# Optimization experiments

Measured on AMD Instinct MI355X. Metric: run time of the kernel, lower is better.

Reference implementation:

```python
import jax, jax.numpy as jnp
import numpy as np

NPOINT = 1024
RADIUS = 0.4
NSAMPLE = 32
BN_EPS = 1e-3  # keras BatchNormalization default epsilon


def _fps(xyz, npoint):
    # xyz: [N,3] -> indices [npoint] via farthest point sampling (seed index 0)
    N = xyz.shape[0]

    def step(carry, _):
        dists, far = carry
        d = jnp.sum((xyz - xyz[far]) ** 2, axis=-1)
        dists = jnp.minimum(dists, d)
        return (dists, jnp.argmax(dists).astype(jnp.int32)), far

    init = (jnp.full((N,), 1e10, dtype=xyz.dtype), jnp.asarray(0, dtype=jnp.int32))
    _, idx = jax.lax.scan(step, init, None, length=npoint)
    return idx


def _ball_query(xyz, new_xyz, radius, nsample):
    # xyz: [N,3], new_xyz: [S,3] -> idx [S,nsample]
    # First up-to-nsample points (in original index order) within radius of each
    # center; slots past the count are filled with the first found index
    # (matching the CUDA query_ball_point semantics).
    N = xyz.shape[0]
    d2 = jnp.sum((new_xyz[:, None, :] - xyz[None, :, :]) ** 2, axis=-1)  # [S,N]
    key = jnp.where(d2 < radius * radius, jnp.arange(N, dtype=jnp.int32), N)
    sk = jnp.sort(key, axis=-1)[:, :nsample]          # first valid indices, padded with N
    first = sk[:, :1]
    first = jnp.where(first < N, first, 0)            # fallback if no neighbor found
    idx = jnp.where(sk < N, sk, first)
    return idx.astype(jnp.int32)


def _gather(pts, idx):
    # pts: [B,N,C], idx: [B,...] -> [B,...,C]
    return jax.vmap(lambda p, i: p[i])(pts, idx)


def _conv_bn_relu(x, W, b, g, be):
    # 1x1 conv over [B,P,S,Cin] + batchnorm (training mode, batch stats) + relu
    y = jnp.einsum('bpsc,co->bpso', x, W) + b
    m = jnp.mean(y, axis=(0, 1, 2))
    v = jnp.var(y, axis=(0, 1, 2))
    y = (y - m) * jax.lax.rsqrt(v + BN_EPS) * g + be
    return jax.nn.relu(y)


def setup_inputs() -> dict:
    key = jax.random.key(0)
    ks = jax.random.split(key, 8)
    B, N, C = 16, 4096, 64
    xyz = jax.random.normal(ks[0], (B, N, 3), dtype=jnp.float32)
    points = jax.random.normal(ks[1], (B, N, C), dtype=jnp.float32)
    chans = [3 + C, 64, 64, 128]
    inp = {'xyz': xyz, 'points': points}
    for i in range(3):
        cin, cout = chans[i], chans[i + 1]
        limit = np.sqrt(6.0 / (cin + cout))  # glorot uniform
        inp[f'W{i}'] = jax.random.uniform(ks[2 + i], (cin, cout), jnp.float32, -limit, limit)
        inp[f'b{i}'] = jnp.zeros((cout,), jnp.float32)
        inp[f'g{i}'] = jnp.ones((cout,), jnp.float32)
        inp[f'be{i}'] = jnp.zeros((cout,), jnp.float32)
    return inp


def reference(xyz, points, W0, b0, g0, be0, W1, b1, g1, be1, W2, b2, g2, be2):
    xyz_c = jax.lax.stop_gradient(xyz)
    fps_idx = jax.vmap(lambda p: _fps(p, NPOINT))(xyz_c)           # [B,NPOINT]
    new_xyz = _gather(xyz, fps_idx)                                 # [B,NPOINT,3]
    idx = jax.vmap(lambda p, c: _ball_query(p, c, RADIUS, NSAMPLE))(
        xyz_c, jax.lax.stop_gradient(new_xyz))                      # [B,NPOINT,NSAMPLE]
    grouped_xyz = _gather(xyz, idx) - new_xyz[:, :, None, :]        # centered local coords
    grouped_points = _gather(points, idx)                           # [B,NPOINT,NSAMPLE,C]
    new_points = jnp.concatenate([grouped_xyz, grouped_points], axis=-1)
    new_points = _conv_bn_relu(new_points, W0, b0, g0, be0)
    new_points = _conv_bn_relu(new_points, W1, b1, g1, be1)
    new_points = _conv_bn_relu(new_points, W2, b2, g2, be2)
    new_points = jnp.max(new_points, axis=2)                        # max-pool over nsample
    return (new_xyz, new_points, idx)
```

## Files before the change

### kernel.cpp

```cpp
#include <hip/hip_runtime.h>

static constexpr int NB      = 16;
static constexpr int NPTS    = 4096;
static constexpr int NPOINTS = 1024;
static constexpr int NSAMP   = 32;
static constexpr int CIN0    = 67;
static constexpr int C0      = 64;
static constexpr int C1      = 64;
static constexpr int C2      = 128;
static constexpr size_t MROWS = (size_t)NB * NPOINTS * NSAMP;
#define RAD2 0.16f
#define BN_EPS 0.001f

__device__ __forceinline__ float4 uld4(const float* __restrict__ p) {
    return *(const float4* __restrict__)p;
}

__device__ __forceinline__ unsigned short f2bf(float f) {
    const unsigned u = __float_as_uint(f);
    return (unsigned short)((u + 0x7fffu + ((u >> 16) & 1u)) >> 16);
}
__device__ __forceinline__ float bf2f(unsigned short h) {
    return __uint_as_float((unsigned)h << 16);
}

template<int CTRL>
__device__ __forceinline__ float dppf(float v) {
    return __int_as_float(__builtin_amdgcn_update_dpp(0, __float_as_int(v),
                                                      CTRL, 0xF, 0xF, false));
}
template<int CTRL>
__device__ __forceinline__ float dpps(float v) {
    return __int_as_float(__builtin_amdgcn_update_dpp(__float_as_int(v), __float_as_int(v),
                                                      CTRL, 0xF, 0xF, false));
}
__device__ __forceinline__ float dpp_sum64(float v) {
    v += dppf<0x111>(v); v += dppf<0x112>(v); v += dppf<0x114>(v); v += dppf<0x118>(v);
    v += dppf<0x142>(v); v += dppf<0x143>(v);
    return v;
}
__device__ __forceinline__ float dpp_max32(float v) {
    v = fmaxf(v, dpps<0x111>(v)); v = fmaxf(v, dpps<0x112>(v));
    v = fmaxf(v, dpps<0x114>(v)); v = fmaxf(v, dpps<0x118>(v));
    v = fmaxf(v, dpps<0x142>(v));
    return v;
}
__device__ __forceinline__ float dpp_min32(float v) {
    v = fminf(v, dpps<0x111>(v)); v = fminf(v, dpps<0x112>(v));
    v = fminf(v, dpps<0x114>(v)); v = fminf(v, dpps<0x118>(v));
    v = fminf(v, dpps<0x142>(v));
    return v;
}
template<int CTRL>
__device__ __forceinline__ void kstep(unsigned long long& k) {
    const unsigned hi = (unsigned)(k >> 32);
    const unsigned lo = (unsigned)(k & 0xffffffffull);
    const unsigned ohi = (unsigned)__builtin_amdgcn_update_dpp((int)hi, (int)hi, CTRL, 0xF, 0xF, false);
    const unsigned olo = (unsigned)__builtin_amdgcn_update_dpp((int)lo, (int)lo, CTRL, 0xF, 0xF, false);
    const unsigned long long ok = ((unsigned long long)ohi << 32) | olo;
    if (ok > k) k = ok;
}

__global__ __launch_bounds__(512) void fps_kernel(const float* __restrict__ xyz,
                                                  float* __restrict__ out_newxyz)
{
    __shared__ float sx[NPTS], sy[NPTS], sz[NPTS];
    __shared__ int   sidx[NPOINTS];
    __shared__ __align__(16) unsigned long long redk[2][8];

    const int b    = blockIdx.x;
    const int tid  = threadIdx.x;
    const int lane = tid & 63;
    const int wv   = tid >> 6;

    const float* base = xyz + (size_t)b * NPTS * 3;
    for (int i = tid; i < NPTS; i += 512) {
        sx[i] = base[i * 3 + 0];
        sy[i] = base[i * 3 + 1];
        sz[i] = base[i * 3 + 2];
    }
    __syncthreads();

    float px[8], py[8], pz[8], dd[8];
#pragma unroll
    for (int j = 0; j < 8; ++j) {
        const int i = tid + j * 512;
        px[j] = sx[i]; py[j] = sy[i]; pz[j] = sz[i];
        dd[j] = 1e10f;
    }

    int   far = 0;
    float fx = sx[0], fy = sy[0], fz = sz[0];
#pragma unroll 1
    for (int it = 0; it < NPOINTS; ++it) {
        if (tid == 0) sidx[it] = far;
        float bv = -1.0f; int bi = 0;
#pragma unroll
        for (int j = 0; j < 8; ++j) {
            const float dx = __fsub_rn(px[j], fx);
            const float dy = __fsub_rn(py[j], fy);
            const float dz = __fsub_rn(pz[j], fz);
            const float d  = __fadd_rn(__fadd_rn(__fmul_rn(dx, dx), __fmul_rn(dy, dy)),
                                       __fmul_rn(dz, dz));
            dd[j] = fminf(dd[j], d);
            if (dd[j] > bv) { bv = dd[j]; bi = tid + j * 512; }
        }
        unsigned long long k = ((unsigned long long)__float_as_uint(bv) << 32)
                             | (unsigned)(4095 - bi);
        kstep<0x111>(k);
        kstep<0x112>(k);
        kstep<0x114>(k);
        kstep<0x118>(k);
        kstep<0x142>(k);
        kstep<0x143>(k);

        const int pb = it & 1;
        if (lane == 63) redk[pb][wv] = k;
        __syncthreads();
// ... 5 lines not shown
        }
        const int ci = 4095 - (int)(unsigned)(ck & 0xffffffffull);
        far = ci;
        fx = sx[ci]; fy = sy[ci]; fz = sz[ci];
    }
    __syncthreads();
    for (int it = tid; it < NPOINTS; it += 512) {
        const int ii = sidx[it];
        float* o = out_newxyz + ((size_t)b * NPOINTS + it) * 3;
        o[0] = sx[ii]; o[1] = sy[ii]; o[2] = sz[ii];
    }
}

__global__ __launch_bounds__(256) void ball_kernel(const float* __restrict__ xyz,
                                                   const float* __restrict__ newxyz,
                                                   float* __restrict__ out_idx_f)
{
    __shared__ int sel[4][NSAMP];
    const int tid  = threadIdx.x;
    const int lane = tid & 63;
    const int widx = tid >> 6;
    const int w = blockIdx.x * 4 + widx;
    const int b = w >> 10;

    const float cx = newxyz[(size_t)w * 3 + 0];
    const float cy = newxyz[(size_t)w * 3 + 1];
    const float cz = newxyz[(size_t)w * 3 + 2];
    const float* base = xyz + (size_t)b * NPTS * 3;

    int total = 0;
    for (int c = 0; c < NPTS / 64 && total < NSAMP; ++c) {
        const int n = c * 64 + lane;
        const float dx = __fsub_rn(cx, base[n * 3 + 0]);
        const float dy = __fsub_rn(cy, base[n * 3 + 1]);
        const float dz = __fsub_rn(cz, base[n * 3 + 2]);
        const float d2 = __fadd_rn(__fadd_rn(__fmul_rn(dx, dx), __fmul_rn(dy, dy)),
                                   __fmul_rn(dz, dz));
        const bool pred = d2 < RAD2;
        const unsigned long long mask = __ballot(pred);
        if (pred) {
            const int pos = total + (int)__popcll(mask & ((1ull << lane) - 1ull));
            if (pos < NSAMP) sel[widx][pos] = n;
        }
        total += (int)__popcll(mask);
    }
    __syncthreads();
    if (lane < NSAMP) {
        const int first = sel[widx][0];
        const int v = (lane < total) ? sel[widx][lane] : first;
        out_idx_f[(size_t)w * NSAMP + lane] = (float)v;
    }
}

__device__ __forceinline__ void stats4(float a0, float a1, float a2, float a3,
                                       float* sa, int lane)
{
    float q0 = a0*a0, q1 = a1*a1, q2 = a2*a2, q3 = a3*a3;
    a0 = dpp_sum64(a0); q0 = dpp_sum64(q0);
    a1 = dpp_sum64(a1); q1 = dpp_sum64(q1);
    a2 = dpp_sum64(a2); q2 = dpp_sum64(q2);
    a3 = dpp_sum64(a3); q3 = dpp_sum64(q3);
    if (lane == 63) {
        sa[0] += a0; sa[1] += q0; sa[2] += a1; sa[3] += q1;
        sa[4] += a2; sa[5] += q2; sa[6] += a3; sa[7] += q3;
    }
}

__global__ __launch_bounds__(256) void preP_kernel(const float* __restrict__ points,
                                                   const float* __restrict__ W0,
                                                   float* __restrict__ P)
{
    const int r = blockIdx.x * 256 + threadIdx.x;
    const float4* pr = (const float4*)(points + (size_t)r * 64);
    float x[64];
#pragma unroll
    for (int j = 0; j < 16; ++j) {
        const float4 v = pr[j];
        x[4*j+0] = v.x; x[4*j+1] = v.y; x[4*j+2] = v.z; x[4*j+3] = v.w;
    }
    float acc[64];
#pragma unroll
    for (int o = 0; o < 64; ++o) acc[o] = 0.f;
#pragma unroll 2
    for (int k = 0; k < 64; ++k) {
        const float xk = x[k];
#pragma unroll
        for (int oc = 0; oc < 16; ++oc) {
            const float4 w4 = uld4(W0 + (3 + k) * 64 + 4 * oc);
            acc[4*oc+0] = fmaf(xk, w4.x, acc[4*oc+0]);
            acc[4*oc+1] = fmaf(xk, w4.y, acc[4*oc+1]);
            acc[4*oc+2] = fmaf(xk, w4.z, acc[4*oc+2]);
            acc[4*oc+3] = fmaf(xk, w4.w, acc[4*oc+3]);
        }
    }
    float4* po = (float4*)(P + (size_t)r * 64);
#pragma unroll
    for (int oc = 0; oc < 16; ++oc)
        po[oc] = make_float4(acc[4*oc+0], acc[4*oc+1], acc[4*oc+2], acc[4*oc+3]);
}

__device__ __forceinline__ void layer0_dedup(
    const float* __restrict__ xyz, const float* __restrict__ P,
    const float* __restrict__ newxyz, const float* __restrict__ idxf,
    const float* __restrict__ W0, const float* __restrict__ b0,
    int r, float* x1)
{
    const int i  = (int)idxf[r];
    const int bb = r >> 15;
    const int pp = (r >> 5) & 1023;
    const float* pz = xyz + ((size_t)bb * NPTS + i) * 3;
    const float* nz = newxyz + ((size_t)bb * NPOINTS + pp) * 3;
    const float r0 = pz[0] - nz[0];
    const float r1 = pz[1] - nz[1];
    const float r2 = pz[2] - nz[2];
    const float4* prow = (const float4*)(P + ((size_t)bb * NPTS + i) * 64);
#pragma unroll
    for (int oc = 0; oc < 16; ++oc) {
        const float4 pv = prow[oc];
        const float4 bv = uld4(b0 + 4 * oc);
        const float4 wa = uld4(W0 + 0 * 64 + 4 * oc);
        const float4 wb = uld4(W0 + 1 * 64 + 4 * oc);
        const float4 wc = uld4(W0 + 2 * 64 + 4 * oc);
        x1[4*oc+0] = fmaf(r0, wa.x, fmaf(r1, wb.x, fmaf(r2, wc.x, bv.x + pv.x)));
        x1[4*oc+1] = fmaf(r0, wa.y, fmaf(r1, wb.y, fmaf(r2, wc.y, bv.y + pv.y)));
        x1[4*oc+2] = fmaf(r0, wa.z, fmaf(r1, wb.z, fmaf(r2, wc.z, bv.z + pv.z)));
        x1[4*oc+3] = fmaf(r0, wa.w, fmaf(r1, wb.w, fmaf(r2, wc.w, bv.w + pv.w)));
    }
}

template<int PHASE>
__global__ __launch_bounds__(256, 2) void passP_kernel(
    const float* __restrict__ xyz, const float* __restrict__ P,
    const float* __restrict__ newxyz, const float* __restrict__ idxf,
    const float* __restrict__ W0, const float* __restrict__ b0,
    const float* __restrict__ W1, const float* __restrict__ b1,
    const float* __restrict__ W2, const float* __restrict__ b2,
    const float* __restrict__ ss0, const float* __restrict__ ss1,
    const float* __restrict__ ss2,
    float* __restrict__ gstats, float* __restrict__ out_np)
{
    constexpr int CS = (PHASE == 2) ? C2 : C0;
    __shared__ float sacc[4][2 * CS];

    const int tid  = threadIdx.x;
    const int lane = tid & 63;
    const int wv   = tid >> 6;

    if constexpr (PHASE <= 2) {
        for (int j = tid; j < 8 * CS; j += 256) (&sacc[0][0])[j] = 0.f;
        __syncthreads();
    }

    const int r = blockIdx.x * 256 + tid;
    float x1[C0];
    layer0_dedup(xyz, P, newxyz, idxf, W0, b0, r, x1);

    if constexpr (PHASE == 0) {
#pragma unroll
        for (int oc = 0; oc < 16; ++oc)
            stats4(x1[4*oc+0], x1[4*oc+1], x1[4*oc+2], x1[4*oc+3], &sacc[wv][8*oc], lane);
    } else {
#pragma unroll
        for (int o = 0; o < C0; ++o)
            x1[o] = fmaxf(0.f, fmaf(x1[o], ss0[o], ss0[64 + o]));

        float y1[C1];
#pragma unroll
        for (int o = 0; o < C1; o += 4) {
            const float4 bv = uld4(b1 + o);
            y1[o] = bv.x; y1[o+1] = bv.y; y1[o+2] = bv.z; y1[o+3] = bv.w;
        }
#pragma unroll 2
        for (int k = 0; k < C0; ++k) {
            const float xk = x1[k];
#pragma unroll
            for (int oc = 0; oc < 16; ++oc) {
                const float4 w4 = uld4(W1 + k * 64 + 4 * oc);
                y1[4*oc+0] = fmaf(xk, w4.x, y1[4*oc+0]);
                y1[4*oc+1] = fmaf(xk, w4.y, y1[4*oc+1]);
                y1[4*oc+2] = fmaf(xk, w4.z, y1[4*oc+2]);
                y1[4*oc+3] = fmaf(xk, w4.w, y1[4*oc+3]);
            }
// ... 3 lines not shown
#pragma unroll
            for (int oc = 0; oc < 16; ++oc)
                stats4(y1[4*oc+0], y1[4*oc+1], y1[4*oc+2], y1[4*oc+3], &sacc[wv][8*oc], lane);
        } else {
#pragma unroll
            for (int o = 0; o < C1; ++o)
                y1[o] = fmaxf(0.f, fmaf(y1[o], ss1[o], ss1[64 + o]));

            float a2[C2];
#pragma unroll
            for (int o = 0; o < C2; o += 4) {
                const float4 bv = uld4(b2 + o);
                a2[o] = bv.x; a2[o+1] = bv.y; a2[o+2] = bv.z; a2[o+3] = bv.w;
            }
#pragma unroll 2
            for (int k = 0; k < C1; ++k) {
                const float xk = y1[k];
#pragma unroll
                for (int o = 0; o < C2; o += 4) {
                    const float4 w4 = uld4(W2 + k * C2 + o);
                    a2[o+0] = fmaf(xk, w4.x, a2[o+0]);
                    a2[o+1] = fmaf(xk, w4.y, a2[o+1]);
                    a2[o+2] = fmaf(xk, w4.z, a2[o+2]);
                    a2[o+3] = fmaf(xk, w4.w, a2[o+3]);
                }
            }

            if constexpr (PHASE == 2) {
#pragma unroll
                for (int o = 0; o < C2; ++o) {
                    const float s = dpp_sum64(a2[o]);
                    const float q = dpp_sum64(a2[o] * a2[o]);
                    if (lane == 63) { sacc[wv][2*o] += s; sacc[wv][2*o+1] += q; }
                }
            } else {
                const int g = r >> 5;
#pragma unroll
                for (int o = 0; o < C2; ++o) {
                    float v = fmaxf(0.f, fmaf(a2[o], ss2[o], ss2[C2 + o]));
                    v = dpp_max32(v);
                    if (lane == 31 || lane == 63) out_np[(size_t)g * C2 + o] = v;
                }
            }
        }
    }

    if constexpr (PHASE <= 2) {
        __syncthreads();
        for (int j = tid; j < 2 * CS; j += 256)
            atomicAdd(&gstats[j], sacc[0][j] + sacc[1][j] + sacc[2][j] + sacc[3][j]);
    }
}

__global__ __launch_bounds__(256, 2) void pass1Y_kernel(
    const float* __restrict__ xyz, const float* __restrict__ P,
    const float* __restrict__ newxyz, const float* __restrict__ idxf,
    const float* __restrict__ W0, const float* __restrict__ b0,
    const float* __restrict__ W1, const float* __restrict__ b1,
    const float* __restrict__ ss0,
    float* __restrict__ gstats, unsigned short* __restrict__ y1b)
{
    __shared__ float sacc[4][2 * C0];

    const int tid  = threadIdx.x;
    const int lane = tid & 63;
    const int wv   = tid >> 6;

    for (int j = tid; j < 8 * C0; j += 256) (&sacc[0][0])[j] = 0.f;
    __syncthreads();

    const int r = blockIdx.x * 256 + tid;
    float x1[C0];
    layer0_dedup(xyz, P, newxyz, idxf, W0, b0, r, x1);
#pragma unroll
    for (int o = 0; o < C0; ++o)
        x1[o] = fmaxf(0.f, fmaf(x1[o], ss0[o], ss0[64 + o]));

    float y1[C1];
#pragma unroll
    for (int o = 0; o < C1; o += 4) {
        const float4 bv = uld4(b1 + o);
        y1[o] = bv.x; y1[o+1] = bv.y; y1[o+2] = bv.z; y1[o+3] = bv.w;
    }
#pragma unroll 2
    for (int k = 0; k < C0; ++k) {
        const float xk = x1[k];
#pragma unroll
        for (int oc = 0; oc < 16; ++oc) {
            const float4 w4 = uld4(W1 + k * 64 + 4 * oc);
            y1[4*oc+0] = fmaf(xk, w4.x, y1[4*oc+0]);
            y1[4*oc+1] = fmaf(xk, w4.y, y1[4*oc+1]);
            y1[4*oc+2] = fmaf(xk, w4.z, y1[4*oc+2]);
            y1[4*oc+3] = fmaf(xk, w4.w, y1[4*oc+3]);
        }
    }

#pragma unroll
    for (int oc = 0; oc < 16; ++oc)
        stats4(y1[4*oc+0], y1[4*oc+1], y1[4*oc+2], y1[4*oc+3], &sacc[wv][8*oc], lane);

    uint4* yo = (uint4*)(y1b + (size_t)r * 64);
#pragma unroll
    for (int gq = 0; gq < 8; ++gq) {
        union { unsigned short u[8]; uint4 v; } pk;
#pragma unroll
        for (int e = 0; e < 8; ++e) pk.u[e] = f2bf(y1[8*gq+e]);
        yo[gq] = pk.v;
    }

    __syncthreads();
    for (int j = tid; j < 2 * C0; j += 256)
        atomicAdd(&gstats[j], sacc[0][j] + sacc[1][j] + sacc[2][j] + sacc[3][j]);
}

__global__ __launch_bounds__(256, 2) void p2Y_kernel(
    const unsigned short* __restrict__ y1b,
    const float* __restrict__ W2, const float* __restrict__ b2,
    const float* __restrict__ ss1,
    float* __restrict__ gstats, float* __restrict__ mnmx)
{
    __shared__ float sacc[4][2 * C2];

    const int tid  = threadIdx.x;
    const int lane = tid & 63;
    const int wv   = tid >> 6;

    for (int j = tid; j < 8 * C2; j += 256) (&sacc[0][0])[j] = 0.f;
    __syncthreads();

    const int r = blockIdx.x * 256 + tid;

    float y1[C1];
    {
        const uint4* yi = (const uint4*)(y1b + (size_t)r * 64);
#pragma unroll
        for (int gq = 0; gq < 8; ++gq) {
            union { uint4 v; unsigned short u[8]; } pk;
            pk.v = yi[gq];
#pragma unroll
            for (int e = 0; e < 8; ++e)
                y1[8*gq+e] = bf2f(pk.u[e]);
        }
    }
#pragma unroll
    for (int o = 0; o < C1; ++o)
        y1[o] = fmaxf(0.f, fmaf(y1[o], ss1[o], ss1[64 + o]));

    float a2[C2];
#pragma unroll
    for (int o = 0; o < C2; o += 4) {
        const float4 bv = uld4(b2 + o);
        a2[o] = bv.x; a2[o+1] = bv.y; a2[o+2] = bv.z; a2[o+3] = bv.w;
    }
#pragma unroll 2
    for (int k = 0; k < C1; ++k) {
        const float xk = y1[k];
#pragma unroll
        for (int o = 0; o < C2; o += 4) {
            const float4 w4 = uld4(W2 + k * C2 + o);
            a2[o+0] = fmaf(xk, w4.x, a2[o+0]);
            a2[o+1] = fmaf(xk, w4.y, a2[o+1]);
            a2[o+2] = fmaf(xk, w4.z, a2[o+2]);
            a2[o+3] = fmaf(xk, w4.w, a2[o+3]);
        }
    }

    const int gbase = blockIdx.x * 8 + 2 * wv;
    float* mb = mnmx + ((size_t)gbase + (lane >> 5)) * 256;
#pragma unroll
    for (int o = 0; o < C2; ++o) {
        const float v = a2[o];
        const float s = dpp_sum64(v);
        const float q = dpp_sum64(v * v);
        const float mn = dpp_min32(v);
        const float mx = dpp_max32(v);
        if (lane == 63) { sacc[wv][2*o] += s; sacc[wv][2*o+1] += q; }
        if (lane == 31 || lane == 63) { mb[o] = mn; mb[128 + o] = mx; }
    }

    __syncthreads();
    for (int j = tid; j < 2 * C2; j += 256)
        atomicAdd(&gstats[j], sacc[0][j] + sacc[1][j] + sacc[2][j] + sacc[3][j]);
}

__global__ __launch_bounds__(256, 2) void passP2mm_kernel(
    const float* __restrict__ xyz, const float* __restrict__ P,
    const float* __restrict__ newxyz, const float* __restrict__ idxf,
    const float* __restrict__ W0, const float* __restrict__ b0,
    const float* __restrict__ W1, const float* __restrict__ b1,
    const float* __restrict__ W2, const float* __restrict__ b2,
    const float* __restrict__ ss0, const float* __restrict__ ss1,
    float* __restrict__ gstats, float* __restrict__ mnmx)
{
    __shared__ float sacc[4][2 * C2];

    const int tid  = threadIdx.x;
    const int lane = tid & 63;
    const int wv   = tid >> 6;

    for (int j = tid; j < 8 * C2; j += 256) (&sacc[0][0])[j] = 0.f;
    __syncthreads();

    const int r = blockIdx.x * 256 + tid;
    float x1[C0];
    layer0_dedup(xyz, P, newxyz, idxf, W0, b0, r, x1);
#pragma unroll
    for (int o = 0; o < C0; ++o)
        x1[o] = fmaxf(0.f, fmaf(x1[o], ss0[o], ss0[64 + o]));

    float y1[C1];
#pragma unroll
    for (int o = 0; o < C1; o += 4) {
        const float4 bv = uld4(b1 + o);
        y1[o] = bv.x; y1[o+1] = bv.y; y1[o+2] = bv.z; y1[o+3] = bv.w;
    }
#pragma unroll 2
    for (int k = 0; k < C0; ++k) {
        const float xk = x1[k];
#pragma unroll
        for (int oc = 0; oc < 16; ++oc) {
            const float4 w4 = uld4(W1 + k * 64 + 4 * oc);
            y1[4*oc+0] = fmaf(xk, w4.x, y1[4*oc+0]);
            y1[4*oc+1] = fmaf(xk, w4.y, y1[4*oc+1]);
            y1[4*oc+2] = fmaf(xk, w4.z, y1[4*oc+2]);
            y1[4*oc+3] = fmaf(xk, w4.w, y1[4*oc+3]);
        }
    }
#pragma unroll
    for (int o = 0; o < C1; ++o)
        y1[o] = fmaxf(0.f, fmaf(y1[o], ss1[o], ss1[64 + o]));

    float a2[C2];
#pragma unroll
    for (int o = 0; o < C2; o += 4) {
        const float4 bv = uld4(b2 + o);
        a2[o] = bv.x; a2[o+1] = bv.y; a2[o+2] = bv.z; a2[o+3] = bv.w;
    }
#pragma unroll 2
    for (int k = 0; k < C1; ++k) {
        const float xk = y1[k];
#pragma unroll
        for (int o = 0; o < C2; o += 4) {
            const float4 w4 = uld4(W2 + k * C2 + o);
            a2[o+0] = fmaf(xk, w4.x, a2[o+0]);
            a2[o+1] = fmaf(xk, w4.y, a2[o+1]);
            a2[o+2] = fmaf(xk, w4.z, a2[o+2]);
            a2[o+3] = fmaf(xk, w4.w, a2[o+3]);
        }
    }

    const int gbase = blockIdx.x * 8 + 2 * wv;
    float* mb = mnmx + ((size_t)gbase + (lane >> 5)) * 256;
#pragma unroll
    for (int o = 0; o < C2; ++o) {
        const float v = a2[o];
        const float s = dpp_sum64(v);
        const float q = dpp_sum64(v * v);
        const float mn = dpp_min32(v);
        const float mx = dpp_max32(v);
        if (lane == 63) { sacc[wv][2*o] += s; sacc[wv][2*o+1] += q; }
        if (lane == 31 || lane == 63) { mb[o] = mn; mb[128 + o] = mx; }
    }

    __syncthreads();
    for (int j = tid; j < 2 * C2; j += 256)
        atomicAdd(&gstats[j], sacc[0][j] + sacc[1][j] + sacc[2][j] + sacc[3][j]);
}

__global__ __launch_bounds__(256) void fin_kernel(const float* __restrict__ mnmx,
                                                  const float* __restrict__ ss2,
                                                  float* __restrict__ out_np)
{
    const int t = blockIdx.x * 256 + threadIdx.x;
    const int g = t >> 7;
    const int o = t & 127;
    const float sc = ss2[o], sh = ss2[C2 + o];
    const float y  = (sc >= 0.f) ? mnmx[(size_t)g * 256 + 128 + o]
                                 : mnmx[(size_t)g * 256 + o];
    out_np[t] = fmaxf(0.f, fmaf(y, sc, sh));
}

template<int PHASE>
__global__ __launch_bounds__(128) void pass_kernel(
    const float* __restrict__ xyz, const float* __restrict__ points,
    const float* __restrict__ newxyz, const float* __restrict__ idxf,
    const float* __restrict__ W0, const float* __restrict__ b0,
    const float* __restrict__ W1, const float* __restrict__ b1,
    const float* __restrict__ W2, const float* __restrict__ b2,
    const float* __restrict__ ss0, const float* __restrict__ ss1,
    const float* __restrict__ ss2,
    float* __restrict__ gstats, float* __restrict__ out_np)
{
    constexpr int CS = (PHASE == 2) ? C2 : C0;
    __shared__ float xld[(PHASE >= 1) ? (64 * 128) : 1];
    __shared__ float sacc[2][2 * CS];

    const int tid  = threadIdx.x;
    const int lane = tid & 63;
    const int wv   = tid >> 6;

    if constexpr (PHASE <= 2) {
        for (int j = tid; j < 2 * 2 * CS; j += 128) (&sacc[0][0])[j] = 0.f;
        __syncthreads();
    }

    const int r  = blockIdx.x * 128 + tid;
    const int i  = (int)idxf[r];
    const int bb = r >> 15;
    const int pp = (r >> 5) & 1023;

    float x[CIN0];
    {
        const float* pz = xyz + ((size_t)bb * NPTS + i) * 3;
        const float* nz = newxyz + ((size_t)bb * NPOINTS + pp) * 3;
        x[0] = pz[0] - nz[0];
        x[1] = pz[1] - nz[1];
        x[2] = pz[2] - nz[2];
        const float4* p4 = (const float4*)(points + ((size_t)bb * NPTS + i) * 64);
#pragma unroll
        for (int j = 0; j < 16; ++j) {
            const float4 v = p4[j];
            x[3+4*j+0] = v.x; x[3+4*j+1] = v.y; x[3+4*j+2] = v.z; x[3+4*j+3] = v.w;
        }
    }

#pragma unroll 1
    for (int oc = 0; oc < 16; ++oc) {
        const float4 bv = uld4(b0 + 4*oc);
        float a0 = bv.x, a1 = bv.y, a2 = bv.z, a3 = bv.w;
#pragma unroll
        for (int k = 0; k < CIN0; ++k) {
            const float4 w4 = uld4(W0 + k*64 + 4*oc);
            a0 = fmaf(x[k], w4.x, a0); a1 = fmaf(x[k], w4.y, a1);
            a2 = fmaf(x[k], w4.z, a2); a3 = fmaf(x[k], w4.w, a3);
// ... 33 lines not shown
        }
#pragma unroll 1
        for (int oc = 0; oc < 16; ++oc) {
            const float4 bv = uld4(b1 + 4*oc);
            float a0 = bv.x, a1 = bv.y, a2 = bv.z, a3 = bv.w;
#pragma unroll
            for (int k = 0; k < 64; ++k) {
                const float xk = xld[k*128 + tid];
                const float4 w4 = uld4(W1 + k*64 + 4*oc);
                a0 = fmaf(xk, w4.x, a0); a1 = fmaf(xk, w4.y, a1);
                a2 = fmaf(xk, w4.z, a2); a3 = fmaf(xk, w4.w, a3);
            }
            const float xc0 = fmaxf(0.f, fmaf(a0, ss1[4*oc+0], ss1[64+4*oc+0]));
            const float xc1 = fmaxf(0.f, fmaf(a1, ss1[4*oc+1], ss1[64+4*oc+1]));
            const float xc2 = fmaxf(0.f, fmaf(a2, ss1[4*oc+2], ss1[64+4*oc+2]));
            const float xc3 = fmaxf(0.f, fmaf(a3, ss1[4*oc+3], ss1[64+4*oc+3]));
#pragma unroll
            for (int o = 0; o < C2; o += 4) {
                const float4 wA = uld4(W2 + (4*oc+0)*C2 + o);
                const float4 wB = uld4(W2 + (4*oc+1)*C2 + o);
                const float4 wC = uld4(W2 + (4*oc+2)*C2 + o);
                const float4 wD = uld4(W2 + (4*oc+3)*C2 + o);
                acc2[o+0] = fmaf(xc0, wA.x, fmaf(xc1, wB.x, fmaf(xc2, wC.x, fmaf(xc3, wD.x, acc2[o+0]))));
                acc2[o+1] = fmaf(xc0, wA.y, fmaf(xc1, wB.y, fmaf(xc2, wC.y, fmaf(xc3, wD.y, acc2[o+1]))));
                acc2[o+2] = fmaf(xc0, wA.z, fmaf(xc1, wB.z, fmaf(xc2, wC.z, fmaf(xc3, wD.z, acc2[o+2]))));
                acc2[o+3] = fmaf(xc0, wA.w, fmaf(xc1, wB.w, fmaf(xc2, wC.w, fmaf(xc3, wD.w, acc2[o+3]))));
            }
        }

        if constexpr (PHASE == 2) {
#pragma unroll
            for (int o = 0; o < C2; ++o) {
                const float s = dpp_sum64(acc2[o]);
                const float q = dpp_sum64(acc2[o] * acc2[o]);
                if (lane == 63) { sacc[wv][2*o] += s; sacc[wv][2*o+1] += q; }
            }
        } else {
            const int g = r >> 5;
#pragma unroll
            for (int o = 0; o < C2; ++o) {
                float v = fmaxf(0.f, fmaf(acc2[o], ss2[o], ss2[C2+o]));
                v = dpp_max32(v);
                if (lane == 31 || lane == 63) out_np[(size_t)g * C2 + o] = v;
            }
        }
    }

    if constexpr (PHASE <= 2) {
        __syncthreads();
        for (int j = tid; j < 2 * CS; j += 128)
            atomicAdd(&gstats[j], sacc[0][j] + sacc[1][j]);
    }
}

template<int C>
__global__ void ss_kernel(const float* __restrict__ gs, const float* __restrict__ g,
                          const float* __restrict__ be, float* __restrict__ ss)
{
    const int o = threadIdx.x;
    const float inv  = 1.0f / (float)MROWS;
    const float mean = gs[2*o] * inv;
    const float var  = fmaxf(0.f, gs[2*o+1] * inv - mean * mean);
    const float sc   = g[o] / sqrtf(var + BN_EPS);
    ss[o]     = sc;
    ss[C + o] = fmaf(-mean, sc, be[o]);
}

__global__ void zero_kernel(float* __restrict__ p) { p[threadIdx.x] = 0.f; }

extern "C" void kernel_launch(void* const* d_in, const int* in_sizes, int n_in,
                              void* d_out, int out_size, void* d_ws, size_t ws_size,
                              hipStream_t stream)
{
    (void)in_sizes; (void)n_in; (void)out_size;
    const float* xyz    = (const float*)d_in[0];
    const float* points = (const float*)d_in[1];
    const float* W0  = (const float*)d_in[2];
    const float* b0  = (const float*)d_in[3];
    const float* g0  = (const float*)d_in[4];
    const float* be0 = (const float*)d_in[5];
    const float* W1  = (const float*)d_in[6];
    const float* b1  = (const float*)d_in[7];
    const float* g1  = (const float*)d_in[8];
    const float* be1 = (const float*)d_in[9];
    const float* W2  = (const float*)d_in[10];
    const float* b2  = (const float*)d_in[11];
    const float* g2  = (const float*)d_in[12];
    const float* be2 = (const float*)d_in[13];

    float* out = (float*)d_out;
    float* out_newxyz = out;
    float* out_newpts = out + (size_t)NB * NPOINTS * 3;
    float* out_idx    = out_newpts + (size_t)NB * NPOINTS * C2;

    float* wsf = (float*)d_ws;
    float* gs0 = wsf + 0;
    float* gs1 = wsf + 128;
    float* gs2 = wsf + 256;
    float* ss0 = wsf + 512;
    float* ss1 = wsf + 640;
    float* ss2 = wsf + 768;
    const size_t PBYTES  = (size_t)NB * NPTS * C0 * 4;
    const size_t MMBYTES = (size_t)NB * NPOINTS * 2 * C2 * 4;
    const size_t YBYTES  = MROWS * C1 * 2;
    float* P    = (float*)((char*)d_ws + 65536);
    float* mnmx = (float*)((char*)d_ws + 65536 + PBYTES);
    unsigned short* y1b = (unsigned short*)((char*)d_ws + 65536 + PBYTES + MMBYTES);

    const bool haveP  = ws_size >= (65536 + PBYTES);
    const bool haveMM = ws_size >= (65536 + PBYTES + MMBYTES);
    const bool haveY  = ws_size >= (65536 + PBYTES + MMBYTES + YBYTES);

    zero_kernel<<<1, 512, 0, stream>>>(wsf);
    fps_kernel<<<NB, 512, 0, stream>>>(xyz, out_newxyz);
    ball_kernel<<<(NB * NPOINTS) / 4, 256, 0, stream>>>(xyz, out_newxyz, out_idx);

    if (haveP) {
        const int grid = (int)(MROWS / 256);
        preP_kernel<<<NB * NPTS / 256, 256, 0, stream>>>(points, W0, P);
        passP_kernel<0><<<grid, 256, 0, stream>>>(xyz, P, out_newxyz, out_idx,
                                                  W0, b0, W1, b1, W2, b2,
                                                  ss0, ss1, ss2, gs0, nullptr);
        ss_kernel<C0><<<1, C0, 0, stream>>>(gs0, g0, be0, ss0);
        if (haveY) {
            pass1Y_kernel<<<grid, 256, 0, stream>>>(xyz, P, out_newxyz, out_idx,
                                                    W0, b0, W1, b1, ss0, gs1, y1b);
            ss_kernel<C1><<<1, C1, 0, stream>>>(gs1, g1, be1, ss1);
            p2Y_kernel<<<grid, 256, 0, stream>>>(y1b, W2, b2, ss1, gs2, mnmx);
            ss_kernel<C2><<<1, C2, 0, stream>>>(gs2, g2, be2, ss2);
            fin_kernel<<<NB * NPOINTS * C2 / 256, 256, 0, stream>>>(mnmx, ss2, out_newpts);
        } else if (haveMM) {
            passP_kernel<1><<<grid, 256, 0, stream>>>(xyz, P, out_newxyz, out_idx,
                                                      W0, b0, W1, b1, W2, b2,
                                                      ss0, ss1, ss2, gs1, nullptr);
            ss_kernel<C1><<<1, C1, 0, stream>>>(gs1, g1, be1, ss1);
            passP2mm_kernel<<<grid, 256, 0, stream>>>(xyz, P, out_newxyz, out_idx,
                                                      W0, b0, W1, b1, W2, b2,
                                                      ss0, ss1, gs2, mnmx);
            ss_kernel<C2><<<1, C2, 0, stream>>>(gs2, g2, be2, ss2);
            fin_kernel<<<NB * NPOINTS * C2 / 256, 256, 0, stream>>>(mnmx, ss2, out_newpts);
        } else {
            passP_kernel<1><<<grid, 256, 0, stream>>>(xyz, P, out_newxyz, out_idx,
                                                      W0, b0, W1, b1, W2, b2,
                                                      ss0, ss1, ss2, gs1, nullptr);
            ss_kernel<C1><<<1, C1, 0, stream>>>(gs1, g1, be1, ss1);
            passP_kernel<2><<<grid, 256, 0, stream>>>(xyz, P, out_newxyz, out_idx,
                                                      W0, b0, W1, b1, W2, b2,
                                                      ss0, ss1, ss2, gs2, nullptr);
            ss_kernel<C2><<<1, C2, 0, stream>>>(gs2, g2, be2, ss2);
            passP_kernel<3><<<grid, 256, 0, stream>>>(xyz, P, out_newxyz, out_idx,
                                                      W0, b0, W1, b1, W2, b2,
                                                      ss0, ss1, ss2, nullptr, out_newpts);
        }
    } else {
        const int grid = (int)(MROWS / 128);
        pass_kernel<0><<<grid, 128, 0, stream>>>(xyz, points, out_newxyz, out_idx,
                                                 W0, b0, W1, b1, W2, b2,
                                                 ss0, ss1, ss2, gs0, nullptr);
        ss_kernel<C0><<<1, C0, 0, stream>>>(gs0, g0, be0, ss0);
        pass_kernel<1><<<grid, 128, 0, stream>>>(xyz, points, out_newxyz, out_idx,
                                                 W0, b0, W1, b1, W2, b2,
                                                 ss0, ss1, ss2, gs1, nullptr);
        ss_kernel<C1><<<1, C1, 0, stream>>>(gs1, g1, be1, ss1);
        pass_kernel<2><<<grid, 128, 0, stream>>>(xyz, points, out_newxyz, out_idx,
                                                 W0, b0, W1, b1, W2, b2,
                                                 ss0, ss1, ss2, gs2, nullptr);
        ss_kernel<C2><<<1, C2, 0, stream>>>(gs2, g2, be2, ss2);
        pass_kernel<3><<<grid, 128, 0, stream>>>(xyz, points, out_newxyz, out_idx,
                                                 W0, b0, W1, b1, W2, b2,
                                                 ss0, ss1, ss2, nullptr, out_newpts);
    }
}
```

Measured before the change: 1.286 ms.

## Fold preP and zeroing into FPS launch, inline BN scale, partial-sum stats

Runs the zeroing and the per-point W0 projection (P) as extra blocks inside the FPS launch, so they overlap the latency-bound FPS blocks instead of running as separate launches. Drops the tiny ss_kernel launches by computing the BN scale and shift inline at the start of each pass and in the final kernel. Adds a dedicated pass0 kernel that only collects layer-0 stats. Replaces the full-wave DPP sums with 8-lane partial sums written to a padded shared array, which removes the shared-memory zeroing and the read-modify-write accumulation. p2Y now splits the 128 output channels into two 64-wide halves to reduce register pressure, and occupancy hints are raised from 2 to 3 or 4 blocks. Costs include redundant BN recomputation per block and the risk of spills from the higher occupancy targets.

```diff
diff --git a/kernel.cpp b/kernel.cpp
--- a/kernel.cpp
+++ b/kernel.cpp
@@ -39,6 +39,14 @@
     v += dppf<0x142>(v); v += dppf<0x143>(v);
     return v;
 }
+__device__ __forceinline__ float dpp_psum8(float v) {
+    v += dppf<0x111>(v); v += dppf<0x112>(v); v += dppf<0x114>(v);
+    return v;
+}
+__device__ __forceinline__ float dpp_psum16(float v) {
+    v += dppf<0x111>(v); v += dppf<0x112>(v); v += dppf<0x114>(v); v += dppf<0x118>(v);
+    return v;
+}
 __device__ __forceinline__ float dpp_max32(float v) {
     v = fmaxf(v, dpps<0x111>(v)); v = fmaxf(v, dpps<0x112>(v));
     v = fmaxf(v, dpps<0x114>(v)); v = fmaxf(v, dpps<0x118>(v));
@@ -62,8 +70,47 @@
 }
 
 __global__ __launch_bounds__(512) void fps_kernel(const float* __restrict__ xyz,
-                                                  float* __restrict__ out_newxyz)
-{
+                                                  float* __restrict__ out_newxyz,
+                                                  float* __restrict__ wsz,
+                                                  const float* __restrict__ points,
+                                                  const float* __restrict__ W0,
+                                                  float* __restrict__ P)
+{
+    if (blockIdx.x == NB) {
+        for (int i = threadIdx.x; i < 1024; i += 512) wsz[i] = 0.f;
+        return;
+    }
+    if (blockIdx.x > NB) {
+        const int r = (blockIdx.x - NB - 1) * 512 + threadIdx.x;
+        const float4* pr = (const float4*)(points + (size_t)r * 64);
+        float x[64];
+#pragma unroll
+        for (int j = 0; j < 16; ++j) {
+            const float4 v = pr[j];
+            x[4*j+0] = v.x; x[4*j+1] = v.y; x[4*j+2] = v.z; x[4*j+3] = v.w;
+        }
+        float acc[64];
+#pragma unroll
+        for (int o = 0; o < 64; ++o) acc[o] = 0.f;
+#pragma unroll 2
+        for (int k = 0; k < 64; ++k) {
+            const float xk = x[k];
+#pragma unroll
+            for (int oc = 0; oc < 16; ++oc) {
+                const float4 w4 = uld4(W0 + (3 + k) * 64 + 4 * oc);
+                acc[4*oc+0] = fmaf(xk, w4.x, acc[4*oc+0]);
+                acc[4*oc+1] = fmaf(xk, w4.y, acc[4*oc+1]);
+                acc[4*oc+2] = fmaf(xk, w4.z, acc[4*oc+2]);
+                acc[4*oc+3] = fmaf(xk, w4.w, acc[4*oc+3]);
+            }
+        }
+        float4* po = (float4*)(P + (size_t)r * 64);
+#pragma unroll
+        for (int oc = 0; oc < 16; ++oc)
+            po[oc] = make_float4(acc[4*oc+0], acc[4*oc+1], acc[4*oc+2], acc[4*oc+3]);
+        return;
+    }
+
     __shared__ float sx[NPTS], sy[NPTS], sz[NPTS];
     __shared__ int   sidx[NPOINTS];
     __shared__ __align__(16) unsigned long long redk[2][8];
@@ -175,6 +222,20 @@
     }
 }
 
+__device__ __forceinline__ void stats4q8(float a0, float a1, float a2, float a3,
+                                         float2* sa, bool wr)
+{
+    float q0 = a0*a0, q1 = a1*a1, q2 = a2*a2, q3 = a3*a3;
+    a0 = dpp_psum8(a0); q0 = dpp_psum8(q0);
+    a1 = dpp_psum8(a1); q1 = dpp_psum8(q1);
+    a2 = dpp_psum8(a2); q2 = dpp_psum8(q2);
+    a3 = dpp_psum8(a3); q3 = dpp_psum8(q3);
+    if (wr) {
+        *(float4*)&sa[0] = make_float4(a0, q0, a1, q1);
+        *(float4*)&sa[2] = make_float4(a2, q2, a3, q3);
+    }
+}
+
 __device__ __forceinline__ void stats4(float a0, float a1, float a2, float a3,
                                        float* sa, int lane)
 {
@@ -251,6 +312,237 @@
     }
 }
 
+template<int C>
+__device__ __forceinline__ void bn_inline(const float* __restrict__ gs,
+                                          const float* __restrict__ g,
+                                          const float* __restrict__ be,
+                                          float* ssl, int tid)
+{
+    if (tid < C) {
+        const float inv  = 1.0f / (float)MROWS;
+        const float mean = gs[2*tid] * inv;
+        const float var  = fmaxf(0.f, gs[2*tid+1] * inv - mean * mean);
+        const float sc   = g[tid] / sqrtf(var + BN_EPS);
+        ssl[tid]     = sc;
+        ssl[C + tid] = fmaf(-mean, sc, be[tid]);
+    }
+}
+
+__global__ __launch_bounds__(256, 4) void pass0_kernel(
+    const float* __restrict__ xyz, const float* __restrict__ P,
+    const float* __restrict__ newxyz, const float* __restrict__ idxf,
+    const float* __restrict__ W0, const float* __restrict__ b0,
+    float* __restrict__ gstats)
+{
+    __shared__ float2 sacc[32][C0 + 1];
+    const int tid  = threadIdx.x;
+    const int lane = tid & 63;
+    const int wv   = tid >> 6;
+    const int slot = wv * 8 + (lane >> 3);
+    const bool wr  = (lane & 7) == 7;
+
+    const int r = blockIdx.x * 256 + tid;
+    float x1[C0];
+    layer0_dedup(xyz, P, newxyz, idxf, W0, b0, r, x1);
+
+#pragma unroll
+    for (int oc = 0; oc < 16; ++oc)
+        stats4q8(x1[4*oc+0], x1[4*oc+1], x1[4*oc+2], x1[4*oc+3], &sacc[slot][4*oc], wr);
+
+    __syncthreads();
+    for (int j = tid; j < C0; j += 256) {
+        float s = 0.f, q = 0.f;
+#pragma unroll
+        for (int v = 0; v < 32; ++v) { s += sacc[v][j].x; q += sacc[v][j].y; }
+        atomicAdd(&gstats[2*j], s);
+        atomicAdd(&gstats[2*j+1], q);
+    }
+}
+
+__global__ __launch_bounds__(256, 3) void pass1Y_kernel(
+    const float* __restrict__ xyz, const float* __restrict__ P,
+    const float* __restrict__ newxyz, const float* __restrict__ idxf,
+    const float* __restrict__ W0, const float* __restrict__ b0,
+    const float* __restrict__ W1, const float* __restrict__ b1,
+    const float* __restrict__ gs0, const float* __restrict__ g0,
+    const float* __restrict__ be0,
+    float* __restrict__ gstats, unsigned short* __restrict__ y1b)
+{
+    __shared__ float2 sacc[32][C0 + 1];
+    __shared__ float ssl[2 * C0];
+    const int tid  = threadIdx.x;
+    const int lane = tid & 63;
+    const int wv   = tid >> 6;
+    const int slot = wv * 8 + (lane >> 3);
+    const bool wr  = (lane & 7) == 7;
+
+    bn_inline<C0>(gs0, g0, be0, ssl, tid);
+    __syncthreads();
+
+    const int r = blockIdx.x * 256 + tid;
+    float x1[C0];
+    layer0_dedup(xyz, P, newxyz, idxf, W0, b0, r, x1);
+#pragma unroll
+    for (int o = 0; o < C0; ++o)
+        x1[o] = fmaxf(0.f, fmaf(x1[o], ssl[o], ssl[64 + o]));
+
+    float y1[C1];
+#pragma unroll
+    for (int o = 0; o < C1; o += 4) {
+        const float4 bv = uld4(b1 + o);
+        y1[o] = bv.x; y1[o+1] = bv.y; y1[o+2] = bv.z; y1[o+3] = bv.w;
+    }
+#pragma unroll 2
+    for (int k = 0; k < C0; ++k) {
+        const float xk = x1[k];
+#pragma unroll
+        for (int oc = 0; oc < 16; ++oc) {
+            const float4 w4 = uld4(W1 + k * 64 + 4 * oc);
+            y1[4*oc+0] = fmaf(xk, w4.x, y1[4*oc+0]);
+            y1[4*oc+1] = fmaf(xk, w4.y, y1[4*oc+1]);
+            y1[4*oc+2] = fmaf(xk, w4.z, y1[4*oc+2]);
+            y1[4*oc+3] = fmaf(xk, w4.w, y1[4*oc+3]);
+        }
+    }
+
+#pragma unroll
+    for (int oc = 0; oc < 16; ++oc)
+        stats4q8(y1[4*oc+0], y1[4*oc+1], y1[4*oc+2], y1[4*oc+3], &sacc[slot][4*oc], wr);
+
+    uint4* yo = (uint4*)(y1b + (size_t)r * 64);
+#pragma unroll
+    for (int gq = 0; gq < 8; ++gq) {
+        union { unsigned short u[8]; uint4 v; } pk;
+#pragma unroll
+        for (int e = 0; e < 8; ++e) pk.u[e] = f2bf(y1[8*gq+e]);
+        yo[gq] = pk.v;
+    }
+
+    __syncthreads();
+    for (int j = tid; j < C0; j += 256) {
+        float s = 0.f, q = 0.f;
+#pragma unroll
+        for (int v = 0; v < 32; ++v) { s += sacc[v][j].x; q += sacc[v][j].y; }
+        atomicAdd(&gstats[2*j], s);
+        atomicAdd(&gstats[2*j+1], q);
+    }
+}
+
+__global__ __launch_bounds__(256, 3) void p2Y_kernel(
+    const unsigned short* __restrict__ y1b,
+    const float* __restrict__ W2, const float* __restrict__ b2,
+    const float* __restrict__ gs1, const float* __restrict__ g1,
+    const float* __restrict__ be1,
+    float* __restrict__ gstats, float2* __restrict__ mnmx)
+{
+    __shared__ float2 sacc[32][C2 + 1];
+    __shared__ float ssl[2 * C1];
+    const int tid  = threadIdx.x;
+    const int lane = tid & 63;
+    const int wv   = tid >> 6;
+    const int slot = wv * 8 + (lane >> 3);
+    const bool wr  = (lane & 7) == 7;
+
+    bn_inline<C1>(gs1, g1, be1, ssl, tid);
+    __syncthreads();
+
+    const int r = blockIdx.x * 256 + tid;
+
+    float y1[C1];
+    {
+        const uint4* yi = (const uint4*)(y1b + (size_t)r * 64);
+#pragma unroll
+        for (int gq = 0; gq < 8; ++gq) {
+            union { uint4 v; unsigned short u[8]; } pk;
+            pk.v = yi[gq];
+#pragma unroll
+            for (int e = 0; e < 8; ++e)
+                y1[8*gq+e] = bf2f(pk.u[e]);
+        }
+    }
+#pragma unroll
+    for (int o = 0; o < C1; ++o)
+        y1[o] = fmaxf(0.f, fmaf(y1[o], ssl[o], ssl[64 + o]));
+
+    const int gbase = blockIdx.x * 8 + 2 * wv;
+    float2* mb = mnmx + ((size_t)gbase + (lane >> 5)) * C2;
+
+#pragma unroll 1
+    for (int to = 0; to < 2; ++to) {
+        const int ob = to * 64;
+        float a2[64];
+#pragma unroll
+        for (int o = 0; o < 64; o += 4) {
+            const float4 bv = uld4(b2 + ob + o);
+            a2[o] = bv.x; a2[o+1] = bv.y; a2[o+2] = bv.z; a2[o+3] = bv.w;
+        }
+#pragma unroll 2
+        for (int k = 0; k < C1; ++k) {
+            const float xk = y1[k];
+#pragma unroll
+            for (int o = 0; o < 64; o += 4) {
+                const float4 w4 = uld4(W2 + k * C2 + ob + o);
+                a2[o+0] = fmaf(xk, w4.x, a2[o+0]);
+                a2[o+1] = fmaf(xk, w4.y, a2[o+1]);
+                a2[o+2] = fmaf(xk, w4.z, a2[o+2]);
+                a2[o+3] = fmaf(xk, w4.w, a2[o+3]);
+            }
+        }
+
+#pragma unroll
+        for (int o = 0; o < 64; ++o) {
+            const float v = a2[o];
+            const float s  = dpp_psum8(v);
+            const float q  = dpp_psum8(v * v);
+            const float mn = dpp_min32(v);
+            const float mx = dpp_max32(v);
+            if (wr) sacc[slot][ob + o] = make_float2(s, q);
+            if (lane == 31 || lane == 63) mb[ob + o] = make_float2(mn, mx);
+        }
+    }
+
+    __syncthreads();
+    for (int j = tid; j < C2; j += 256) {
+        float s = 0.f, q = 0.f;
+#pragma unroll
+        for (int v = 0; v < 32; ++v) { s += sacc[v][j].x; q += sacc[v][j].y; }
+        atomicAdd(&gstats[2*j], s);
+        atomicAdd(&gstats[2*j+1], q);
+    }
+}
+
+__global__ __launch_bounds__(256) void finY_kernel(const float2* __restrict__ mnmx,
+                                                   const float* __restrict__ gs2,
+                                                   const float* __restrict__ g2,
+                                                   const float* __restrict__ be2,
+                                                   float* __restrict__ out_np)
+{
+    const int t = blockIdx.x * 256 + threadIdx.x;
+    const int g = t >> 7;
+    const int o = t & 127;
+    const float inv  = 1.0f / (float)MROWS;
+    const float mean = gs2[2*o] * inv;
+    const float var  = fmaxf(0.f, gs2[2*o+1] * inv - mean * mean);
+    const float sc   = g2[o] / sqrtf(var + BN_EPS);
+    const float sh   = fmaf(-mean, sc, be2[o]);
+    const float2 mm  = mnmx[(size_t)g * C2 + o];
+    const float y    = (sc >= 0.f) ? mm.y : mm.x;
+    out_np[t] = fmaxf(0.f, fmaf(y, sc, sh));
+}
+
+template<int C>
+__global__ void ss_kernel(const float* __restrict__ gs, const float* __restrict__ g,
+                          const float* __restrict__ be, float* __restrict__ ss)
+{
+    const int o = threadIdx.x;
+    const float inv  = 1.0f / (float)MROWS;
+    const float mean = gs[2*o] * inv;
+    const float var  = fmaxf(0.f, gs[2*o+1] * inv - mean * mean);
+    const float sc   = g[o] / sqrtf(var + BN_EPS);
+    ss[o]     = sc;
+    ss[C + o] = fmaf(-mean, sc, be[o]);
+}
+
 template<int PHASE>
 __global__ __launch_bounds__(256, 2) void passP_kernel(
     const float* __restrict__ xyz, const float* __restrict__ P,
@@ -360,234 +652,6 @@
     }
 }
 
-__global__ __launch_bounds__(256, 2) void pass1Y_kernel(
-    const float* __restrict__ xyz, const float* __restrict__ P,
-    const float* __restrict__ newxyz, const float* __restrict__ idxf,
-    const float* __restrict__ W0, const float* __restrict__ b0,
-    const float* __restrict__ W1, const float* __restrict__ b1,
-    const float* __restrict__ ss0,
-    float* __restrict__ gstats, unsigned short* __restrict__ y1b)
-{
-    __shared__ float sacc[4][2 * C0];
-
-    const int tid  = threadIdx.x;
-    const int lane = tid & 63;
-    const int wv   = tid >> 6;
-
-    for (int j = tid; j < 8 * C0; j += 256) (&sacc[0][0])[j] = 0.f;
-    __syncthreads();
-
-    const int r = blockIdx.x * 256 + tid;
-    float x1[C0];
-    layer0_dedup(xyz, P, newxyz, idxf, W0, b0, r, x1);
-#pragma unroll
-    for (int o = 0; o < C0; ++o)
-        x1[o] = fmaxf(0.f, fmaf(x1[o], ss0[o], ss0[64 + o]));
-
-    float y1[C1];
-#pragma unroll
-    for (int o = 0; o < C1; o += 4) {
-        const float4 bv = uld4(b1 + o);
-        y1[o] = bv.x; y1[o+1] = bv.y; y1[o+2] = bv.z; y1[o+3] = bv.w;
-    }
-#pragma unroll 2
-    for (int k = 0; k < C0; ++k) {
-        const float xk = x1[k];
-#pragma unroll
-        for (int oc = 0; oc < 16; ++oc) {
-            const float4 w4 = uld4(W1 + k * 64 + 4 * oc);
-            y1[4*oc+0] = fmaf(xk, w4.x, y1[4*oc+0]);
-            y1[4*oc+1] = fmaf(xk, w4.y, y1[4*oc+1]);
-            y1[4*oc+2] = fmaf(xk, w4.z, y1[4*oc+2]);
-            y1[4*oc+3] = fmaf(xk, w4.w, y1[4*oc+3]);
-        }
-    }
-
-#pragma unroll
-    for (int oc = 0; oc < 16; ++oc)
-        stats4(y1[4*oc+0], y1[4*oc+1], y1[4*oc+2], y1[4*oc+3], &sacc[wv][8*oc], lane);
-
-    uint4* yo = (uint4*)(y1b + (size_t)r * 64);
-#pragma unroll
-    for (int gq = 0; gq < 8; ++gq) {
-        union { unsigned short u[8]; uint4 v; } pk;
-#pragma unroll
-        for (int e = 0; e < 8; ++e) pk.u[e] = f2bf(y1[8*gq+e]);
-        yo[gq] = pk.v;
-    }
-
-    __syncthreads();
-    for (int j = tid; j < 2 * C0; j += 256)
-        atomicAdd(&gstats[j], sacc[0][j] + sacc[1][j] + sacc[2][j] + sacc[3][j]);
-}
-
-__global__ __launch_bounds__(256, 2) void p2Y_kernel(
-    const unsigned short* __restrict__ y1b,
-    const float* __restrict__ W2, const float* __restrict__ b2,
-    const float* __restrict__ ss1,
-    float* __restrict__ gstats, float* __restrict__ mnmx)
-{
-    __shared__ float sacc[4][2 * C2];
-
-    const int tid  = threadIdx.x;
-    const int lane = tid & 63;
-    const int wv   = tid >> 6;
-
-    for (int j = tid; j < 8 * C2; j += 256) (&sacc[0][0])[j] = 0.f;
-    __syncthreads();
-
-    const int r = blockIdx.x * 256 + tid;
-
-    float y1[C1];
-    {
-        const uint4* yi = (const uint4*)(y1b + (size_t)r * 64);
-#pragma unroll
-        for (int gq = 0; gq < 8; ++gq) {
-            union { uint4 v; unsigned short u[8]; } pk;
-            pk.v = yi[gq];
-#pragma unroll
-            for (int e = 0; e < 8; ++e)
-                y1[8*gq+e] = bf2f(pk.u[e]);
-        }
-    }
-#pragma unroll
-    for (int o = 0; o < C1; ++o)
-        y1[o] = fmaxf(0.f, fmaf(y1[o], ss1[o], ss1[64 + o]));
-
-    float a2[C2];
-#pragma unroll
-    for (int o = 0; o < C2; o += 4) {
-        const float4 bv = uld4(b2 + o);
-        a2[o] = bv.x; a2[o+1] = bv.y; a2[o+2] = bv.z; a2[o+3] = bv.w;
-    }
-#pragma unroll 2
-    for (int k = 0; k < C1; ++k) {
-        const float xk = y1[k];
-#pragma unroll
-        for (int o = 0; o < C2; o += 4) {
-            const float4 w4 = uld4(W2 + k * C2 + o);
-            a2[o+0] = fmaf(xk, w4.x, a2[o+0]);
-            a2[o+1] = fmaf(xk, w4.y, a2[o+1]);
-            a2[o+2] = fmaf(xk, w4.z, a2[o+2]);
-            a2[o+3] = fmaf(xk, w4.w, a2[o+3]);
-        }
-    }
-
-    const int gbase = blockIdx.x * 8 + 2 * wv;
-    float* mb = mnmx + ((size_t)gbase + (lane >> 5)) * 256;
-#pragma unroll
-    for (int o = 0; o < C2; ++o) {
-        const float v = a2[o];
-        const float s = dpp_sum64(v);
-        const float q = dpp_sum64(v * v);
-        const float mn = dpp_min32(v);
-        const float mx = dpp_max32(v);
-        if (lane == 63) { sacc[wv][2*o] += s; sacc[wv][2*o+1] += q; }
-        if (lane == 31 || lane == 63) { mb[o] = mn; mb[128 + o] = mx; }
-    }
-
-    __syncthreads();
-    for (int j = tid; j < 2 * C2; j += 256)
-        atomicAdd(&gstats[j], sacc[0][j] + sacc[1][j] + sacc[2][j] + sacc[3][j]);
-}
-
-__global__ __launch_bounds__(256, 2) void passP2mm_kernel(
-    const float* __restrict__ xyz, const float* __restrict__ P,
-    const float* __restrict__ newxyz, const float* __restrict__ idxf,
-    const float* __restrict__ W0, const float* __restrict__ b0,
-    const float* __restrict__ W1, const float* __restrict__ b1,
-    const float* __restrict__ W2, const float* __restrict__ b2,
-    const float* __restrict__ ss0, const float* __restrict__ ss1,
-    float* __restrict__ gstats, float* __restrict__ mnmx)
-{
-    __shared__ float sacc[4][2 * C2];
-
-    const int tid  = threadIdx.x;
-    const int lane = tid & 63;
-    const int wv   = tid >> 6;
-
-    for (int j = tid; j < 8 * C2; j += 256) (&sacc[0][0])[j] = 0.f;
-    __syncthreads();
-
-    const int r = blockIdx.x * 256 + tid;
-    float x1[C0];
-    layer0_dedup(xyz, P, newxyz, idxf, W0, b0, r, x1);
-#pragma unroll
-    for (int o = 0; o < C0; ++o)
-        x1[o] = fmaxf(0.f, fmaf(x1[o], ss0[o], ss0[64 + o]));
-
-    float y1[C1];
-#pragma unroll
-    for (int o = 0; o < C1; o += 4) {
-        const float4 bv = uld4(b1 + o);
-        y1[o] = bv.x; y1[o+1] = bv.y; y1[o+2] = bv.z; y1[o+3] = bv.w;
-    }
-#pragma unroll 2
-    for (int k = 0; k < C0; ++k) {
-        const float xk = x1[k];
-#pragma unroll
-        for (int oc = 0; oc < 16; ++oc) {
-            const float4 w4 = uld4(W1 + k * 64 + 4 * oc);
-            y1[4*oc+0] = fmaf(xk, w4.x, y1[4*oc+0]);
-            y1[4*oc+1] = fmaf(xk, w4.y, y1[4*oc+1]);
-            y1[4*oc+2] = fmaf(xk, w4.z, y1[4*oc+2]);
-            y1[4*oc+3] = fmaf(xk, w4.w, y1[4*oc+3]);
-        }
-    }
-#pragma unroll
-    for (int o = 0; o < C1; ++o)
-        y1[o] = fmaxf(0.f, fmaf(y1[o], ss1[o], ss1[64 + o]));
-
-    float a2[C2];
-#pragma unroll
-    for (int o = 0; o < C2; o += 4) {
-        const float4 bv = uld4(b2 + o);
-        a2[o] = bv.x; a2[o+1] = bv.y; a2[o+2] = bv.z; a2[o+3] = bv.w;
-    }
-#pragma unroll 2
-    for (int k = 0; k < C1; ++k) {
-        const float xk = y1[k];
-#pragma unroll
-        for (int o = 0; o < C2; o += 4) {
-            const float4 w4 = uld4(W2 + k * C2 + o);
-            a2[o+0] = fmaf(xk, w4.x, a2[o+0]);
-            a2[o+1] = fmaf(xk, w4.y, a2[o+1]);
-            a2[o+2] = fmaf(xk, w4.z, a2[o+2]);
-            a2[o+3] = fmaf(xk, w4.w, a2[o+3]);
-        }
-    }
-
-    const int gbase = blockIdx.x * 8 + 2 * wv;
-    float* mb = mnmx + ((size_t)gbase + (lane >> 5)) * 256;
-#pragma unroll
-    for (int o = 0; o < C2; ++o) {
-        const float v = a2[o];
-        const float s = dpp_sum64(v);
-        const float q = dpp_sum64(v * v);
-        const float mn = dpp_min32(v);
-        const float mx = dpp_max32(v);
-        if (lane == 63) { sacc[wv][2*o] += s; sacc[wv][2*o+1] += q; }
-        if (lane == 31 || lane == 63) { mb[o] = mn; mb[128 + o] = mx; }
-    }
-
-    __syncthreads();
-    for (int j = tid; j < 2 * C2; j += 256)
-        atomicAdd(&gstats[j], sacc[0][j] + sacc[1][j] + sacc[2][j] + sacc[3][j]);
-}
-
-__global__ __launch_bounds__(256) void fin_kernel(const float* __restrict__ mnmx,
-                                                  const float* __restrict__ ss2,
-                                                  float* __restrict__ out_np)
-{
-    const int t = blockIdx.x * 256 + threadIdx.x;
-    const int g = t >> 7;
-    const int o = t & 127;
-    const float sc = ss2[o], sh = ss2[C2 + o];
-    const float y  = (sc >= 0.f) ? mnmx[(size_t)g * 256 + 128 + o]
-                                 : mnmx[(size_t)g * 256 + o];
-    out_np[t] = fmaxf(0.f, fmaf(y, sc, sh));
-}
-
 template<int PHASE>
 __global__ __launch_bounds__(128) void pass_kernel(
     const float* __restrict__ xyz, const float* __restrict__ points,
@@ -727,21 +791,6 @@
             atomicAdd(&gstats[j], sacc[0][j] + sacc[1][j]);
     }
 }
-
-template<int C>
-__global__ void ss_kernel(const float* __restrict__ gs, const float* __restrict__ g,
-                          const float* __restrict__ be, float* __restrict__ ss)
-{
-    const int o = threadIdx.x;
-    const float inv  = 1.0f / (float)MROWS;
-    const float mean = gs[2*o] * inv;
-    const float var  = fmaxf(0.f, gs[2*o+1] * inv - mean * mean);
-    const float sc   = g[o] / sqrtf(var + BN_EPS);
-    ss[o]     = sc;
-    ss[C + o] = fmaf(-mean, sc, be[o]);
-}
-
-__global__ void zero_kernel(float* __restrict__ p) { p[threadIdx.x] = 0.f; }
 
 extern "C" void kernel_launch(void* const* d_in, const int* in_sizes, int n_in,
                               void* d_out, int out_size, void* d_ws, size_t ws_size,
@@ -786,47 +835,39 @@
     const bool haveMM = ws_size >= (65536 + PBYTES + MMBYTES);
     const bool haveY  = ws_size >= (65536 + PBYTES + MMBYTES + YBYTES);
 
-    zero_kernel<<<1, 512, 0, stream>>>(wsf);
-    fps_kernel<<<NB, 512, 0, stream>>>(xyz, out_newxyz);
+    const int frontGrid = NB + 1 + (haveP ? (NB * NPTS / 512) : 0);
+    fps_kernel<<<frontGrid, 512, 0, stream>>>(xyz, out_newxyz, wsf, points, W0, P);
     ball_kernel<<<(NB * NPOINTS) / 4, 256, 0, stream>>>(xyz, out_newxyz, out_idx);
 
-    if (haveP) {
+    if (haveY) {
         const int grid = (int)(MROWS / 256);
-        preP_kernel<<<NB * NPTS / 256, 256, 0, stream>>>(points, W0, P);
+        pass0_kernel<<<grid, 256, 0, stream>>>(xyz, P, out_newxyz, out_idx,
+                                               W0, b0, gs0);
+        pass1Y_kernel<<<grid, 256, 0, stream>>>(xyz, P, out_newxyz, out_idx,
+                                                W0, b0, W1, b1, gs0, g0, be0,
+                                                gs1, y1b);
+        p2Y_kernel<<<grid, 256, 0, stream>>>(y1b, W2, b2, gs1, g1, be1,
+                                             gs2, (float2*)mnmx);
+        finY_kernel<<<NB * NPOINTS * C2 / 256, 256, 0, stream>>>((const float2*)mnmx,
+                                                                 gs2, g2, be2, out_newpts);
+    } else if (haveP) {
+        const int grid = (int)(MROWS / 256);
         passP_kernel<0><<<grid, 256, 0, stream>>>(xyz, P, out_newxyz, out_idx,
                                                   W0, b0, W1, b1, W2, b2,
                                                   ss0, ss1, ss2, gs0, nullptr);
         ss_kernel<C0><<<1, C0, 0, stream>>>(gs0, g0, be0, ss0);
-        if (haveY) {
-            pass1Y_kernel<<<grid, 256, 0, stream>>>(xyz, P, out_newxyz, out_idx,
-                                                    W0, b0, W1, b1, ss0, gs1, y1b);
-            ss_kernel<C1><<<1, C1, 0, stream>>>(gs1, g1, be1, ss1);
-            p2Y_kernel<<<grid, 256, 0, stream>>>(y1b, W2, b2, ss1, gs2, mnmx);
-            ss_kernel<C2><<<1, C2, 0, stream>>>(gs2, g2, be2, ss2);
-            fin_kernel<<<NB * NPOINTS * C2 / 256, 256, 0, stream>>>(mnmx, ss2, out_newpts);
-        } else if (haveMM) {
-            passP_kernel<1><<<grid, 256, 0, stream>>>(xyz, P, out_newxyz, out_idx,
-                                                      W0, b0, W1, b1, W2, b2,
-                                                      ss0, ss1, ss2, gs1, nullptr);
-            ss_kernel<C1><<<1, C1, 0, stream>>>(gs1, g1, be1, ss1);
-            passP2mm_kernel<<<grid, 256, 0, stream>>>(xyz, P, out_newxyz, out_idx,
-                                                      W0, b0, W1, b1, W2, b2,
-                                                      ss0, ss1, gs2, mnmx);
-            ss_kernel<C2><<<1, C2, 0, stream>>>(gs2, g2, be2, ss2);
-            fin_kernel<<<NB * NPOINTS * C2 / 256, 256, 0, stream>>>(mnmx, ss2, out_newpts);
-        } else {
-            passP_kernel<1><<<grid, 256, 0, stream>>>(xyz, P, out_newxyz, out_idx,
-                                                      W0, b0, W1, b1, W2, b2,
-                                                      ss0, ss1, ss2, gs1, nullptr);
-            ss_kernel<C1><<<1, C1, 0, stream>>>(gs1, g1, be1, ss1);
-            passP_kernel<2><<<grid, 256, 0, stream>>>(xyz, P, out_newxyz, out_idx,
-                                                      W0, b0, W1, b1, W2, b2,
-                                                      ss0, ss1, ss2, gs2, nullptr);
-            ss_kernel<C2><<<1, C2, 0, stream>>>(gs2, g2, be2, ss2);
-            passP_kernel<3><<<grid, 256, 0, stream>>>(xyz, P, out_newxyz, out_idx,
-                                                      W0, b0, W1, b1, W2, b2,
-                                                      ss0, ss1, ss2, nullptr, out_newpts);
-        }
+        passP_kernel<1><<<grid, 256, 0, stream>>>(xyz, P, out_newxyz, out_idx,
+                                                  W0, b0, W1, b1, W2, b2,
+                                                  ss0, ss1, ss2, gs1, nullptr);
+        ss_kernel<C1><<<1, C1, 0, stream>>>(gs1, g1, be1, ss1);
+        passP_kernel<2><<<grid, 256, 0, stream>>>(xyz, P, out_newxyz, out_idx,
+                                                  W0, b0, W1, b1, W2, b2,
+                                                  ss0, ss1, ss2, gs2, nullptr);
+        ss_kernel<C2><<<1, C2, 0, stream>>>(gs2, g2, be2, ss2);
+        passP_kernel<3><<<grid, 256, 0, stream>>>(xyz, P, out_newxyz, out_idx,
+                                                  W0, b0, W1, b1, W2, b2,
+                                                  ss0, ss1, ss2, nullptr, out_newpts);
+        (void)haveMM;
     } else {
         const int grid = (int)(MROWS / 128);
         pass_kernel<0><<<grid, 128, 0, stream>>>(xyz, points, out_newxyz, out_idx,
```

After: 1.304 ms. Within noise of the previous version (+1.3%).
